# Performance work log

Hardware: AMD Instinct MI355X
Metric: run time of the kernel (lower is better)

## Reference

```python
import jax, jax.numpy as jnp
import numpy as np

FEAT_DIM = 256
DEPTH = 2
N = 8192


def setup_inputs() -> dict:
    key = jax.random.key(0)
    ks = jax.random.split(key, 5)
    bd = 1.0 / FEAT_DIM
    X = jax.random.normal(ks[0], (N, FEAT_DIM), dtype=jnp.float32)
    coefs = jax.random.normal(ks[1], (N,), dtype=jnp.float32)
    linear = jax.random.uniform(ks[2], (DEPTH, FEAT_DIM), minval=-bd, maxval=bd, dtype=jnp.float32)
    dirv = jax.random.uniform(ks[3], (DEPTH, FEAT_DIM), minval=-bd, maxval=bd, dtype=jnp.float32)
    feat = jax.random.uniform(ks[4], (DEPTH, FEAT_DIM), minval=-bd, maxval=bd, dtype=jnp.float32)
    return {"X": X, "coefs": coefs, "linear": linear, "dirv": dirv, "feat": feat}


def reference(X, coefs, linear, dirv, feat):
    # coefs is unused: the torch forward returns before the coef_embed branch.
    emb = X
    n = X.shape[0]
    for i in range(linear.shape[0]):  # depth: small fixed loop
        # torch: emb3[j,a,k] = linear[a]*emb[j,k]; q = sum_a feat[a]*emb3 = (feat.linear)*emb
        a = jnp.dot(feat[i], linear[i])
        b = jnp.dot(dirv[i], linear[i])
        q = a * emb                      # [N, F]
        k = b * emb                      # [N, F]
        k_norm = k / jnp.linalg.norm(k)  # global Frobenius norm, as torch.norm(k)
        inner = jnp.sum(q * k_norm, axis=-1)            # [N]
        scale = jnp.where(inner <= 0, inner, 0.0)       # inner * (inner<=0)
        emb = q - scale[:, None] * k_norm
        # graph_block: X_up[i] = X[i] + (X@X[i]) @ (X - X[i]) / N
        # == X + (S@X - rowsum(S)*X)/N with S = X X^T
        S = emb @ emb.T                                 # [N, N]
        emb = emb + (S @ emb - jnp.sum(S, axis=1, keepdims=True) * emb) / n
    out = jnp.mean(emb @ emb.T, axis=-1)[:-1]           # [N-1]
    return out
```

## Files before the change

kernel.cpp:

```cpp
#include <hip/hip_runtime.h>
#include <math.h>

constexpr int NROW = 8192;
constexpr int FD   = 256;
constexpr int NZ   = 16;

typedef unsigned short u16;
typedef __attribute__((ext_vector_type(8))) short short8;
typedef __attribute__((ext_vector_type(4))) float f32x4;


__device__ __forceinline__ float f_of(float nj, float A, float B, float AB) {
    float inner = AB * nj;
    return A - (inner <= 0.f ? inner : 0.f) * B;
}
__device__ __forceinline__ float wred(float s) {
    #pragma unroll
    for (int off = 32; off; off >>= 1) s += __shfl_xor(s, off);
    return s;
}
__device__ __forceinline__ float dot4(float4 a, float4 b) {
    return a.x*b.x + a.y*b.y + a.z*b.z + a.w*b.w;
}
__device__ __forceinline__ u16 f2bf(float x) {
    unsigned int u = __float_as_uint(x);
    u = (u + 0x7FFFu + ((u >> 16) & 1u)) >> 16;
    return (u16)u;
}

__global__ void k_norm(const float* __restrict__ in, float* __restrict__ nrm,
                       float* __restrict__ fpart) {
    __shared__ float bs[4];
    int wave = threadIdx.x >> 6, lane = threadIdx.x & 63;
    int row = blockIdx.x * 4 + wave;
    const float4 v = *(const float4*)&in[(size_t)row * FD + lane * 4];
    float s = wred(dot4(v, v));
    if (lane == 0) { nrm[row] = s; bs[wave] = s; }
    __syncthreads();
    if (threadIdx.x == 0) fpart[blockIdx.x] = bs[0] + bs[1] + bs[2] + bs[3];
}

__global__ void __launch_bounds__(256, 2)
k_prep(const float* __restrict__ X, const float* __restrict__ nrm0,
       const float* __restrict__ fpart, const float* __restrict__ linear,
       const float* __restrict__ dirv, const float* __restrict__ feat,
       float* __restrict__ scal, float* __restrict__ f0,
       u16* __restrict__ Rbf, u16* __restrict__ Rt, float* __restrict__ cpart) {
    __shared__ u16 T[32][264];
    __shared__ float cred[4][256];
    __shared__ float l[256];
    __shared__ float ff[32];
    __shared__ float sdot[4];
    const int tid = threadIdx.x;
    const int r0 = blockIdx.x * 32;
    if (tid < 64) {
        for (int i = 0; i < 2; ++i) {
            float pa = 0.f, pb = 0.f;
            for (int k = tid; k < FD; k += 64) {
                float ll = linear[i*FD + k];
                pa += feat[i*FD + k] * ll;
                pb += dirv[i*FD + k] * ll;
            }
            pa = wred(pa); pb = wred(pb);
            if (tid == 0) { sdot[i] = pa; sdot[2 + i] = pb; }
        }
    }
    float s = 0.f;
    #pragma unroll
    for (int k = 0; k < 8; ++k) s += fpart[tid + k * 256];
    l[tid] = s;
    __syncthreads();
    for (int off = 128; off; off >>= 1) {
        if (tid < off) l[tid] += l[tid + off];
        __syncthreads();
    }
    const float F2 = l[0];
    const float a = sdot[0], b = sdot[2];
    const float sb = (b > 0.f) ? 1.f : ((b < 0.f) ? -1.f : 0.f);
    const float B = sb / sqrtf(F2);
    const float A = a, AB = a * B;
    if (blockIdx.x == 0 && tid == 0) {
        scal[0] = sdot[0]; scal[1] = sdot[1]; scal[2] = sdot[2]; scal[3] = sdot[3];
        scal[4] = A; scal[5] = B; scal[6] = AB; scal[7] = F2;
    }
    if (tid < 32) {
        float f = f_of(nrm0[r0 + tid], A, B, AB);
        ff[tid] = f;
        f0[r0 + tid] = f;
    }
    __syncthreads();
    const int cg0 = (tid & 63) * 4;
    const int rg = tid >> 6;
    float4 csum = make_float4(0.f, 0.f, 0.f, 0.f);
    #pragma unroll
    for (int i = 0; i < 8; ++i) {
        int row = rg * 8 + i;
        float4 v = *(const float4*)&X[(size_t)(r0 + row) * FD + cg0];
        float f = ff[row];
        v.x *= f; v.y *= f; v.z *= f; v.w *= f;
        csum.x += v.x; csum.y += v.y; csum.z += v.z; csum.w += v.w;
        unsigned lo = (unsigned)f2bf(v.x) | ((unsigned)f2bf(v.y) << 16);
        unsigned hi = (unsigned)f2bf(v.z) | ((unsigned)f2bf(v.w) << 16);
        uint2 pk = make_uint2(lo, hi);
        *(uint2*)&Rbf[(size_t)(r0 + row) * FD + cg0] = pk;
        *(uint2*)&T[row][cg0] = pk;
    }
    *(float4*)&cred[rg][cg0] = csum;
    __syncthreads();
    cpart[(size_t)blockIdx.x * FD + tid] =
        cred[0][tid] + cred[1][tid] + cred[2][tid] + cred[3][tid];
    const int c = tid;
    #pragma unroll
    for (int ch = 0; ch < 4; ++ch) {
        unsigned w0 = (unsigned)T[ch*8+0][c] | ((unsigned)T[ch*8+1][c] << 16);
        unsigned w1 = (unsigned)T[ch*8+2][c] | ((unsigned)T[ch*8+3][c] << 16);
        unsigned w2 = (unsigned)T[ch*8+4][c] | ((unsigned)T[ch*8+5][c] << 16);
        unsigned w3 = (unsigned)T[ch*8+6][c] | ((unsigned)T[ch*8+7][c] << 16);
        uint4 o = make_uint4(w0, w1, w2, w3);
        *(uint4*)&Rt[(size_t)c * NROW + r0 + ch * 8] = o;
    }
}

__global__ void __launch_bounds__(256, 2)
k_gram(const u16* __restrict__ Rt, float* __restrict__ Gp) {
    const int bi = blockIdx.x, bj = blockIdx.y, z = blockIdx.z;
    const int tid = threadIdx.x, w = tid >> 6, lane = tid & 63;
    const int l15 = lane & 15, quad = lane >> 4;
    const int m0 = bi * 64 + (w & 1) * 32;
    const int n0 = bj * 64 + (w >> 1) * 32;
    const size_t kbase = (size_t)z * 512 + quad * 8;
    const u16* am0 = Rt + (size_t)(m0 + l15) * NROW + kbase;
    const u16* am1 = am0 + (size_t)16 * NROW;
    const u16* bn0 = Rt + (size_t)(n0 + l15) * NROW + kbase;
    const u16* bn1 = bn0 + (size_t)16 * NROW;
    f32x4 acc[2][2] = {};
    #pragma unroll
    for (int s = 0; s < 16; ++s) {
        int ko = s * 32;
        short8 a0 = *(const short8*)(am0 + ko);
        short8 a1 = *(const short8*)(am1 + ko);
        short8 b0 = *(const short8*)(bn0 + ko);
        short8 b1 = *(const short8*)(bn1 + ko);
        acc[0][0] = __builtin_amdgcn_mfma_f32_16x16x32_bf16(a0, b0, acc[0][0], 0, 0, 0);
        acc[0][1] = __builtin_amdgcn_mfma_f32_16x16x32_bf16(a0, b1, acc[0][1], 0, 0, 0);
        acc[1][0] = __builtin_amdgcn_mfma_f32_16x16x32_bf16(a1, b0, acc[1][0], 0, 0, 0);
        acc[1][1] = __builtin_amdgcn_mfma_f32_16x16x32_bf16(a1, b1, acc[1][1], 0, 0, 0);
    }
    float* gz = Gp + (size_t)z * (FD * FD);
    #pragma unroll
    for (int mi = 0; mi < 2; ++mi)
        #pragma unroll
        for (int ni = 0; ni < 2; ++ni)
            #pragma unroll
            for (int r = 0; r < 4; ++r)
                gz[(size_t)(m0 + mi*16 + quad*4 + r) * FD + n0 + ni*16 + l15] =
                    acc[mi][ni][r];
}

__global__ void k_gred(const float* __restrict__ Gp, u16* __restrict__ Gbf,
                       const float* __restrict__ cpart, float* __restrict__ cpart2) {
    size_t e0 = (size_t)blockIdx.x * 256 + threadIdx.x;
    float s = 0.f;
    #pragma unroll
    for (int z = 0; z < NZ; ++z) s += Gp[(size_t)z * (FD * FD) + e0];
    Gbf[e0] = f2bf(s);
    if (blockIdx.x < 16) {
        float c = 0.f;
        #pragma unroll
        for (int k = 0; k < 16; ++k)
            c += cpart[(size_t)(blockIdx.x * 16 + k) * FD + threadIdx.x];
        cpart2[(size_t)blockIdx.x * FD + threadIdx.x] = c;
    }
}

__global__ void __launch_bounds__(256, 2)
k_apply(const float* __restrict__ X, const u16* __restrict__ Rbf,
        const u16* __restrict__ Gbf, const float* __restrict__ f0,
        const float* __restrict__ cpart2, float* __restrict__ emb,
        float* __restrict__ nrm1, float* __restrict__ fpart1,
        float* __restrict__ cpart1, float* __restrict__ wpart1) {
    __shared__ float Sl[16][260];
    __shared__ float csh[FD];
    __shared__ float u0s[16], ffs[16], nrs[16];
    __shared__ float nw16[16][16];
    const int tid = threadIdx.x, w = tid >> 6, lane = tid & 63;
    const int l15 = lane & 15, quad = lane >> 4;
    const int r0 = blockIdx.x * 16;

    {
        float s = 0.f;
        #pragma unroll
        for (int g = 0; g < 16; ++g) s += cpart2[(size_t)g * FD + tid];
        csh[tid] = s;
    }
    if (tid < 16) ffs[tid] = f0[r0 + tid];
    __syncthreads();
    #pragma unroll
    for (int jj = 0; jj < 4; ++jj) {
        int row = w * 4 + jj;
        float4 xv = *(const float4*)&X[(size_t)(r0 + row) * FD + lane * 4];
        float4 cv = *(const float4*)&csh[lane * 4];
        float t = wred(dot4(xv, cv));
        if (lane == 0) u0s[row] = ffs[row] * t;
    }
    const u16* ap = Rbf + (size_t)(r0 + l15) * FD + quad * 8;
    const int n0w = w * 64;
    const u16* bp = Gbf + (size_t)(n0w + l15) * FD + quad * 8;
    f32x4 acc[4] = {};
    #pragma unroll
    for (int s = 0; s < 8; ++s) {
        int ko = s * 32;
        short8 a0 = *(const short8*)(ap + ko);
        short8 b0 = *(const short8*)(bp + ko);
        short8 b1 = *(const short8*)(bp + 16 * FD + ko);
        short8 b2 = *(const short8*)(bp + 32 * FD + ko);
        short8 b3 = *(const short8*)(bp + 48 * FD + ko);
        acc[0] = __builtin_amdgcn_mfma_f32_16x16x32_bf16(a0, b0, acc[0], 0, 0, 0);
        acc[1] = __builtin_amdgcn_mfma_f32_16x16x32_bf16(a0, b1, acc[1], 0, 0, 0);
        acc[2] = __builtin_amdgcn_mfma_f32_16x16x32_bf16(a0, b2, acc[2], 0, 0, 0);
        acc[3] = __builtin_amdgcn_mfma_f32_16x16x32_bf16(a0, b3, acc[3], 0, 0, 0);
    }
    #pragma unroll
    for (int ni = 0; ni < 4; ++ni)
        #pragma unroll
        for (int r = 0; r < 4; ++r)
            Sl[quad*4 + r][n0w + ni*16 + l15] = acc[ni][r];
    __syncthreads();
    const float invN = 1.0f / NROW;
    float er[16];
    float csum = 0.f;
    #pragma unroll
    for (int j = 0; j < 16; ++j) {
        float x = X[(size_t)(r0 + j) * FD + tid];
        float rv = ffs[j] * x;
        float e = rv + (Sl[j][tid] - u0s[j] * rv) * invN;
        emb[(size_t)(r0 + j) * FD + tid] = e;
        er[j] = e;
        csum += e;
        Sl[j][tid] = e * e;
    }
    __syncthreads();
    {
        int row = tid & 15, q = tid >> 4;
        float pn = 0.f;
        #pragma unroll
        for (int i = 0; i < 16; ++i) pn += Sl[row][q * 16 + i];
        nw16[row][q] = pn;
    }
    __syncthreads();
    if (tid < 16) {
        float nn = 0.f;
        #pragma unroll
        for (int q = 0; q < 16; ++q) nn += nw16[tid][q];
        nrm1[r0 + tid] = nn;
        nrs[tid] = nn;
    }
    __syncthreads();
    float wsum = 0.f;
    #pragma unroll
    for (int j = 0; j < 16; ++j) wsum += nrs[j] * er[j];
    cpart1[(size_t)blockIdx.x * FD + tid] = csum;
    wpart1[(size_t)blockIdx.x * FD + tid] = wsum;
    if (tid == 0) {
        float fp = 0.f;
        #pragma unroll
        for (int j = 0; j < 16; ++j) fp += nrs[j];
        fpart1[blockIdx.x] = fp;
    }
}

__device__ __forceinline__ void red1_scal(const float* fpart1, const float* scal,
                                          float* l, float& A, float& B, float& AB,
                                          float& kap) {
    int tid = threadIdx.x;
    l[tid] = fpart1[tid] + fpart1[tid + 256];
    __syncthreads();
    for (int off = 128; off; off >>= 1) {
        if (tid < off) l[tid] += l[tid + off];
        __syncthreads();
    }
    float F2 = l[0];
    float a = scal[1], b = scal[3];
    float sb = (b > 0.f) ? 1.f : ((b < 0.f) ? -1.f : 0.f);
    B = sb / sqrtf(F2);
    A = a; AB = a * B;
    kap = (AB <= 0.f) ? AB * B : 0.f;
    __syncthreads();
}

__global__ void k_sv(const float* __restrict__ fpart1, const float* __restrict__ scal,
                     const float* __restrict__ cpart1, const float* __restrict__ wpart1,
                     float* __restrict__ svec, float* __restrict__ scal2) {
    __shared__ float l[256];
    float A1, B1, AB1, kap;
    red1_scal(fpart1, scal, l, A1, B1, AB1, kap);
    int tid = threadIdx.x;
    int col = blockIdx.x * 4 + (tid >> 6);
    int lane = tid & 63;
    float cs = 0.f, wsm = 0.f;
    #pragma unroll
    for (int b = lane; b < 512; b += 64) {
        cs  += cpart1[(size_t)b * FD + col];
        wsm += wpart1[(size_t)b * FD + col];
    }
    #pragma unroll
    for (int off = 32; off; off >>= 1) {
        cs  += __shfl_down(cs, off);
        wsm += __shfl_down(wsm, off);
    }
    if (lane == 0) svec[col] = A1 * cs - kap * wsm;
    if (blockIdx.x == 0 && tid == 0) { scal2[0] = A1; scal2[1] = kap; }
}

__global__ void k_uv(const float* __restrict__ emb, const float* __restrict__ nrm1,
                     const float* __restrict__ scal2, const float* __restrict__ svec,
                     float* __restrict__ u, float* __restrict__ vpart) {
    __shared__ float ssh[FD];
    __shared__ float uf[16];
    const int tid = threadIdx.x;
    const int r0 = blockIdx.x * 16;
    const float A1 = scal2[0], kap = scal2[1];
    ssh[tid] = svec[tid];
    __syncthreads();
    const int wave = tid >> 6, lane = tid & 63;
    float4 sv = *(const float4*)&ssh[lane*4];
    #pragma unroll
    for (int jj = 0; jj < 4; ++jj) {
        int row = r0 + wave * 4 + jj;
        float4 ev = *(const float4*)&emb[(size_t)row * FD + lane*4];
        float s = wred(dot4(ev, sv));
        if (lane == 0) {
            float f = A1 - kap * nrm1[row];
            float uj = f * s;
            u[row] = uj;
            uf[wave*4 + jj] = uj * f;
        }
    }
    __syncthreads();
    float vp = 0.f;
    #pragma unroll
    for (int j = 0; j < 16; ++j)
        vp += uf[j] * emb[(size_t)(r0 + j) * FD + tid];
    vpart[(size_t)blockIdx.x * FD + tid] = vp;
}

__global__ void k_vred(const float* __restrict__ part, float* __restrict__ vec) {
    int tid = threadIdx.x;
    int col = blockIdx.x * 4 + (tid >> 6);
    int lane = tid & 63;
    float s = 0.f;
    #pragma unroll
    for (int b = 0; b < 8; ++b) s += part[(size_t)(b * 64 + lane) * FD + col];
    #pragma unroll
    for (int off = 32; off; off >>= 1) s += __shfl_down(s, off);
    if (lane == 0) vec[col] = s;
}

__global__ void k_out(const float* __restrict__ emb, const float* __restrict__ nrm1,
                      const float* __restrict__ scal2, const float* __restrict__ vvec,
                      const float* __restrict__ u, float* __restrict__ out) {
    __shared__ float vsh[FD];
    const int tid = threadIdx.x;
    const int r0 = blockIdx.x * 16;
    const float A1 = scal2[0], kap = scal2[1];
    vsh[tid] = vvec[tid];
    __syncthreads();
    const int wave = tid >> 6, lane = tid & 63;
    const float invN = 1.0f / NROW;
    float4 vv = *(const float4*)&vsh[lane*4];
    #pragma unroll
    for (int jj = 0; jj < 4; ++jj) {
        int row = r0 + wave * 4 + jj;
        float4 ev = *(const float4*)&emb[(size_t)row * FD + lane*4];
        float s = wred(dot4(ev, vv));
        if (lane == 0 && row < NROW - 1) {
            float f = A1 - kap * nrm1[row];
            float uj = u[row];
            out[row] = (uj + (f * s - uj * uj) * invN) * invN;
        }
    }
}

extern "C" void kernel_launch(void* const* d_in, const int* in_sizes, int n_in,
                              void* d_out, int out_size, void* d_ws, size_t ws_size,
                              hipStream_t stream) {
    const float* X      = (const float*)d_in[0];
    const float* linear = (const float*)d_in[2];
    const float* dirv   = (const float*)d_in[3];
    const float* feat   = (const float*)d_in[4];
    float* out = (float*)d_out;

    char* ws = (char*)d_ws;
    float* scal   = (float*)(ws + 0);
    float* scal2  = (float*)(ws + 128);
    float* fpart  = (float*)(ws + 4096);
    float* nrm0   = (float*)(ws + 12288);
    float* nrm1   = (float*)(ws + 45056);
    float* f0     = (float*)(ws + 77824);
    float* fpart1 = (float*)(ws + 110592);
    float* svec   = (float*)(ws + 112640);
    float* vvec   = (float*)(ws + 113664);
    float* cpart2 = (float*)(ws + 114688);
    float* cpart  = (float*)(ws + 131072);
    float* cpart1 = (float*)(ws + 393216);
    float* wpart1 = (float*)(ws + 917504);
    float* vpart  = (float*)(ws + 1441792);
    u16*   Gbf    = (u16*)  (ws + 1966080);
    u16*   Rbf    = (u16*)  (ws + 2097152);
    u16*   Rt     = (u16*)  (ws + 6291456);
    float* Gp     = (float*)(ws + 10485760);
    float* emb    = (float*)(ws + 14680064);
    float* u      = (float*)(ws + 23068672);

    k_norm<<<NROW/4, 256, 0, stream>>>(X, nrm0, fpart);
    k_prep<<<256, 256, 0, stream>>>(X, nrm0, fpart, linear, dirv, feat,
                                    scal, f0, Rbf, Rt, cpart);
    k_gram<<<dim3(4,4,NZ), 256, 0, stream>>>(Rt, Gp);
    k_gred<<<256, 256, 0, stream>>>(Gp, Gbf, cpart, cpart2);
    k_apply<<<512, 256, 0, stream>>>(X, Rbf, Gbf, f0, cpart2, emb, nrm1,
                                     fpart1, cpart1, wpart1);
    k_sv<<<64, 256, 0, stream>>>(fpart1, scal, cpart1, wpart1, svec, scal2);
    k_uv<<<NROW/16, 256, 0, stream>>>(emb, nrm1, scal2, svec, u, vpart);
    k_vred<<<64, 256, 0, stream>>>(vpart, vvec);
    k_out<<<NROW/16, 256, 0, stream>>>(emb, nrm1, scal2, vvec, u, out);
}
```

Baseline: 122.5 us.

## Pad transposed buffer, cache X in LDS, fold reductions and replace vred with atomics

```diff
diff --git a/kernel.cpp b/kernel.cpp
--- a/kernel.cpp
+++ b/kernel.cpp
@@ -1,9 +1,10 @@
 #include <hip/hip_runtime.h>
 #include <math.h>
 
-constexpr int NROW = 8192;
-constexpr int FD   = 256;
-constexpr int NZ   = 16;
+constexpr int NROW  = 8192;
+constexpr int FD    = 256;
+constexpr int NZ    = 16;
+constexpr int RT_LD = NROW + 32;
 
 typedef unsigned short u16;
 typedef __attribute__((ext_vector_type(8))) short short8;
@@ -30,14 +31,23 @@
 
 __global__ void k_norm(const float* __restrict__ in, float* __restrict__ nrm,
                        float* __restrict__ fpart) {
-    __shared__ float bs[4];
+    __shared__ float bs[16];
     int wave = threadIdx.x >> 6, lane = threadIdx.x & 63;
-    int row = blockIdx.x * 4 + wave;
-    const float4 v = *(const float4*)&in[(size_t)row * FD + lane * 4];
-    float s = wred(dot4(v, v));
-    if (lane == 0) { nrm[row] = s; bs[wave] = s; }
-    __syncthreads();
-    if (threadIdx.x == 0) fpart[blockIdx.x] = bs[0] + bs[1] + bs[2] + bs[3];
+    int base = blockIdx.x * 16 + wave * 4;
+    #pragma unroll
+    for (int jj = 0; jj < 4; ++jj) {
+        int row = base + jj;
+        const float4 v = *(const float4*)&in[(size_t)row * FD + lane * 4];
+        float s = wred(dot4(v, v));
+        if (lane == 0) { nrm[row] = s; bs[wave * 4 + jj] = s; }
+    }
+    __syncthreads();
+    if (threadIdx.x == 0) {
+        float t = 0.f;
+        #pragma unroll
+        for (int i = 0; i < 16; ++i) t += bs[i];
+        fpart[blockIdx.x] = t;
+    }
 }
 
 __global__ void __launch_bounds__(256, 2)
@@ -65,10 +75,7 @@
             if (tid == 0) { sdot[i] = pa; sdot[2 + i] = pb; }
         }
     }
-    float s = 0.f;
-    #pragma unroll
-    for (int k = 0; k < 8; ++k) s += fpart[tid + k * 256];
-    l[tid] = s;
+    l[tid] = fpart[tid] + fpart[tid + 256];
     __syncthreads();
     for (int off = 128; off; off >>= 1) {
         if (tid < off) l[tid] += l[tid + off];
@@ -91,33 +98,33 @@
     __syncthreads();
     const int cg0 = (tid & 63) * 4;
     const int rg = tid >> 6;
-    float4 csum = make_float4(0.f, 0.f, 0.f, 0.f);
+    float4 csumv = make_float4(0.f, 0.f, 0.f, 0.f);
     #pragma unroll
     for (int i = 0; i < 8; ++i) {
         int row = rg * 8 + i;
         float4 v = *(const float4*)&X[(size_t)(r0 + row) * FD + cg0];
         float f = ff[row];
         v.x *= f; v.y *= f; v.z *= f; v.w *= f;
-        csum.x += v.x; csum.y += v.y; csum.z += v.z; csum.w += v.w;
+        csumv.x += v.x; csumv.y += v.y; csumv.z += v.z; csumv.w += v.w;
         unsigned lo = (unsigned)f2bf(v.x) | ((unsigned)f2bf(v.y) << 16);
         unsigned hi = (unsigned)f2bf(v.z) | ((unsigned)f2bf(v.w) << 16);
         uint2 pk = make_uint2(lo, hi);
         *(uint2*)&Rbf[(size_t)(r0 + row) * FD + cg0] = pk;
         *(uint2*)&T[row][cg0] = pk;
     }
-    *(float4*)&cred[rg][cg0] = csum;
+    *(float4*)&cred[rg][cg0] = csumv;
     __syncthreads();
     cpart[(size_t)blockIdx.x * FD + tid] =
         cred[0][tid] + cred[1][tid] + cred[2][tid] + cred[3][tid];
-    const int c = tid;
-    #pragma unroll
-    for (int ch = 0; ch < 4; ++ch) {
-        unsigned w0 = (unsigned)T[ch*8+0][c] | ((unsigned)T[ch*8+1][c] << 16);
-        unsigned w1 = (unsigned)T[ch*8+2][c] | ((unsigned)T[ch*8+3][c] << 16);
-        unsigned w2 = (unsigned)T[ch*8+4][c] | ((unsigned)T[ch*8+5][c] << 16);
-        unsigned w3 = (unsigned)T[ch*8+6][c] | ((unsigned)T[ch*8+7][c] << 16);
-        uint4 o = make_uint4(w0, w1, w2, w3);
-        *(uint4*)&Rt[(size_t)c * NROW + r0 + ch * 8] = o;
+    #pragma unroll
+    for (int it = 0; it < 4; ++it) {
+        int c  = it * 64 + (tid >> 2);
+        int rb = (tid & 3) * 8;
+        unsigned w0 = (unsigned)T[rb+0][c] | ((unsigned)T[rb+1][c] << 16);
+        unsigned w1 = (unsigned)T[rb+2][c] | ((unsigned)T[rb+3][c] << 16);
+        unsigned w2 = (unsigned)T[rb+4][c] | ((unsigned)T[rb+5][c] << 16);
+        unsigned w3 = (unsigned)T[rb+6][c] | ((unsigned)T[rb+7][c] << 16);
+        *(uint4*)&Rt[(size_t)c * RT_LD + r0 + rb] = make_uint4(w0, w1, w2, w3);
     }
 }
 
@@ -129,10 +136,10 @@
     const int m0 = bi * 64 + (w & 1) * 32;
     const int n0 = bj * 64 + (w >> 1) * 32;
     const size_t kbase = (size_t)z * 512 + quad * 8;
-    const u16* am0 = Rt + (size_t)(m0 + l15) * NROW + kbase;
-    const u16* am1 = am0 + (size_t)16 * NROW;
-    const u16* bn0 = Rt + (size_t)(n0 + l15) * NROW + kbase;
-    const u16* bn1 = bn0 + (size_t)16 * NROW;
+    const u16* am0 = Rt + (size_t)(m0 + l15) * RT_LD + kbase;
+    const u16* am1 = am0 + (size_t)16 * RT_LD;
+    const u16* bn0 = Rt + (size_t)(n0 + l15) * RT_LD + kbase;
+    const u16* bn1 = bn0 + (size_t)16 * RT_LD;
     f32x4 acc[2][2] = {};
     #pragma unroll
     for (int s = 0; s < 16; ++s) {
@@ -158,28 +165,29 @@
 }
 
 __global__ void k_gred(const float* __restrict__ Gp, u16* __restrict__ Gbf,
-                       const float* __restrict__ cpart, float* __restrict__ cpart2) {
+                       const float* __restrict__ cpart, float* __restrict__ csum) {
     size_t e0 = (size_t)blockIdx.x * 256 + threadIdx.x;
     float s = 0.f;
     #pragma unroll
     for (int z = 0; z < NZ; ++z) s += Gp[(size_t)z * (FD * FD) + e0];
     Gbf[e0] = f2bf(s);
-    if (blockIdx.x < 16) {
+    if (blockIdx.x == 0) {
         float c = 0.f;
-        #pragma unroll
-        for (int k = 0; k < 16; ++k)
-            c += cpart[(size_t)(blockIdx.x * 16 + k) * FD + threadIdx.x];
-        cpart2[(size_t)blockIdx.x * FD + threadIdx.x] = c;
+        #pragma unroll 16
+        for (int k = 0; k < 256; ++k)
+            c += cpart[(size_t)k * FD + threadIdx.x];
+        csum[threadIdx.x] = c;
     }
 }
 
 __global__ void __launch_bounds__(256, 2)
 k_apply(const float* __restrict__ X, const u16* __restrict__ Rbf,
         const u16* __restrict__ Gbf, const float* __restrict__ f0,
-        const float* __restrict__ cpart2, float* __restrict__ emb,
+        const float* __restrict__ csum, float* __restrict__ emb,
         float* __restrict__ nrm1, float* __restrict__ fpart1,
         float* __restrict__ cpart1, float* __restrict__ wpart1) {
     __shared__ float Sl[16][260];
+    __shared__ float Xs[16][256];
     __shared__ float csh[FD];
     __shared__ float u0s[16], ffs[16], nrs[16];
     __shared__ float nw16[16][16];
@@ -187,18 +195,14 @@
     const int l15 = lane & 15, quad = lane >> 4;
     const int r0 = blockIdx.x * 16;
 
-    {
-        float s = 0.f;
-        #pragma unroll
-        for (int g = 0; g < 16; ++g) s += cpart2[(size_t)g * FD + tid];
-        csh[tid] = s;
-    }
+    csh[tid] = csum[tid];
     if (tid < 16) ffs[tid] = f0[r0 + tid];
     __syncthreads();
     #pragma unroll
     for (int jj = 0; jj < 4; ++jj) {
         int row = w * 4 + jj;
         float4 xv = *(const float4*)&X[(size_t)(r0 + row) * FD + lane * 4];
+        *(float4*)&Xs[row][lane * 4] = xv;
         float4 cv = *(const float4*)&csh[lane * 4];
         float t = wred(dot4(xv, cv));
         if (lane == 0) u0s[row] = ffs[row] * t;
@@ -228,15 +232,15 @@
     __syncthreads();
     const float invN = 1.0f / NROW;
     float er[16];
-    float csum = 0.f;
+    float cs = 0.f;
     #pragma unroll
     for (int j = 0; j < 16; ++j) {
-        float x = X[(size_t)(r0 + j) * FD + tid];
+        float x = Xs[j][tid];
         float rv = ffs[j] * x;
         float e = rv + (Sl[j][tid] - u0s[j] * rv) * invN;
         emb[(size_t)(r0 + j) * FD + tid] = e;
         er[j] = e;
-        csum += e;
+        cs += e;
         Sl[j][tid] = e * e;
     }
     __syncthreads();
@@ -259,7 +263,7 @@
     float wsum = 0.f;
     #pragma unroll
     for (int j = 0; j < 16; ++j) wsum += nrs[j] * er[j];
-    cpart1[(size_t)blockIdx.x * FD + tid] = csum;
+    cpart1[(size_t)blockIdx.x * FD + tid] = cs;
     wpart1[(size_t)blockIdx.x * FD + tid] = wsum;
     if (tid == 0) {
         float fp = 0.f;
@@ -290,8 +294,10 @@
 
 __global__ void k_sv(const float* __restrict__ fpart1, const float* __restrict__ scal,
                      const float* __restrict__ cpart1, const float* __restrict__ wpart1,
-                     float* __restrict__ svec, float* __restrict__ scal2) {
+                     float* __restrict__ svec, float* __restrict__ scal2,
+                     float* __restrict__ vvec) {
     __shared__ float l[256];
+    if (blockIdx.x == 1) vvec[threadIdx.x] = 0.f;
     float A1, B1, AB1, kap;
     red1_scal(fpart1, scal, l, A1, B1, AB1, kap);
     int tid = threadIdx.x;
@@ -312,48 +318,38 @@
     if (blockIdx.x == 0 && tid == 0) { scal2[0] = A1; scal2[1] = kap; }
 }
 
-__global__ void k_uv(const float* __restrict__ emb, const float* __restrict__ nrm1,
-                     const float* __restrict__ scal2, const float* __restrict__ svec,
-                     float* __restrict__ u, float* __restrict__ vpart) {
-    __shared__ float ssh[FD];
+__global__ void __launch_bounds__(256)
+k_uv(const float* __restrict__ emb, const float* __restrict__ nrm1,
+     const float* __restrict__ scal2, const float* __restrict__ svec,
+     float* __restrict__ u, float* __restrict__ vvec) {
+    __shared__ float red[4][16];
     __shared__ float uf[16];
-    const int tid = threadIdx.x;
+    const int tid = threadIdx.x, w = tid >> 6, lane = tid & 63;
     const int r0 = blockIdx.x * 16;
     const float A1 = scal2[0], kap = scal2[1];
-    ssh[tid] = svec[tid];
-    __syncthreads();
-    const int wave = tid >> 6, lane = tid & 63;
-    float4 sv = *(const float4*)&ssh[lane*4];
-    #pragma unroll
-    for (int jj = 0; jj < 4; ++jj) {
-        int row = r0 + wave * 4 + jj;
-        float4 ev = *(const float4*)&emb[(size_t)row * FD + lane*4];
-        float s = wred(dot4(ev, sv));
-        if (lane == 0) {
-            float f = A1 - kap * nrm1[row];
-            float uj = f * s;
-            u[row] = uj;
-            uf[wave*4 + jj] = uj * f;
-        }
+    const float svt = svec[tid];
+    float er[16];
+    #pragma unroll
+    for (int j = 0; j < 16; ++j)
+        er[j] = emb[(size_t)(r0 + j) * FD + tid];
+    #pragma unroll
+    for (int j = 0; j < 16; ++j) {
+        float v = wred(er[j] * svt);
+        if (lane == 0) red[w][j] = v;
+    }
+    __syncthreads();
+    if (tid < 16) {
+        float s = red[0][tid] + red[1][tid] + red[2][tid] + red[3][tid];
+        float f = A1 - kap * nrm1[r0 + tid];
+        float uj = f * s;
+        u[r0 + tid] = uj;
+        uf[tid] = uj * f;
     }
     __syncthreads();
     float vp = 0.f;
     #pragma unroll
-    for (int j = 0; j < 16; ++j)
-        vp += uf[j] * emb[(size_t)(r0 + j) * FD + tid];
-    vpart[(size_t)blockIdx.x * FD + tid] = vp;
-}
-
-__global__ void k_vred(const float* __restrict__ part, float* __restrict__ vec) {
-    int tid = threadIdx.x;
-    int col = blockIdx.x * 4 + (tid >> 6);
-    int lane = tid & 63;
-    float s = 0.f;
-    #pragma unroll
-    for (int b = 0; b < 8; ++b) s += part[(size_t)(b * 64 + lane) * FD + col];
-    #pragma unroll
-    for (int off = 32; off; off >>= 1) s += __shfl_down(s, off);
-    if (lane == 0) vec[col] = s;
+    for (int j = 0; j < 16; ++j) vp += uf[j] * er[j];
+    atomicAdd(&vvec[tid], vp);
 }
 
 __global__ void k_out(const float* __restrict__ emb, const float* __restrict__ nrm1,
@@ -400,27 +396,25 @@
     float* fpart1 = (float*)(ws + 110592);
     float* svec   = (float*)(ws + 112640);
     float* vvec   = (float*)(ws + 113664);
-    float* cpart2 = (float*)(ws + 114688);
+    float* csum   = (float*)(ws + 114688);
     float* cpart  = (float*)(ws + 131072);
     float* cpart1 = (float*)(ws + 393216);
     float* wpart1 = (float*)(ws + 917504);
-    float* vpart  = (float*)(ws + 1441792);
     u16*   Gbf    = (u16*)  (ws + 1966080);
     u16*   Rbf    = (u16*)  (ws + 2097152);
     u16*   Rt     = (u16*)  (ws + 6291456);
-    float* Gp     = (float*)(ws + 10485760);
-    float* emb    = (float*)(ws + 14680064);
-    float* u      = (float*)(ws + 23068672);
-
-    k_norm<<<NROW/4, 256, 0, stream>>>(X, nrm0, fpart);
+    float* Gp     = (float*)(ws + 10502144);
+    float* emb    = (float*)(ws + 14696448);
+    float* u      = (float*)(ws + 23084928);
+
+    k_norm<<<NROW/16, 256, 0, stream>>>(X, nrm0, fpart);
     k_prep<<<256, 256, 0, stream>>>(X, nrm0, fpart, linear, dirv, feat,
                                     scal, f0, Rbf, Rt, cpart);
     k_gram<<<dim3(4,4,NZ), 256, 0, stream>>>(Rt, Gp);
-    k_gred<<<256, 256, 0, stream>>>(Gp, Gbf, cpart, cpart2);
-    k_apply<<<512, 256, 0, stream>>>(X, Rbf, Gbf, f0, cpart2, emb, nrm1,
+    k_gred<<<256, 256, 0, stream>>>(Gp, Gbf, cpart, csum);
+    k_apply<<<512, 256, 0, stream>>>(X, Rbf, Gbf, f0, csum, emb, nrm1,
                                      fpart1, cpart1, wpart1);
-    k_sv<<<64, 256, 0, stream>>>(fpart1, scal, cpart1, wpart1, svec, scal2);
-    k_uv<<<NROW/16, 256, 0, stream>>>(emb, nrm1, scal2, svec, u, vpart);
-    k_vred<<<64, 256, 0, stream>>>(vpart, vvec);
+    k_sv<<<64, 256, 0, stream>>>(fpart1, scal, cpart1, wpart1, svec, scal2, vvec);
+    k_uv<<<NROW/16, 256, 0, stream>>>(emb, nrm1, scal2, svec, u, vvec);
     k_out<<<NROW/16, 256, 0, stream>>>(emb, nrm1, scal2, vvec, u, out);
 }
```

Result: slower. 137.5 us (+12.2%).
